# Kernel optimization log

Measured on AMD Instinct MI355X. Metric: run time of the kernel, lower is better.

The kernel has to match this reference:

```python
import jax, jax.numpy as jnp
import numpy as np

H = 8  # num_attention_heads
DH = 64  # attention_head_size
D = H * DH  # hidden_size = 512
LN_EPS = 1e-6


def setup_inputs() -> dict:
    key = jax.random.key(0)
    ks = jax.random.split(key, 12)
    B, L = 32, 196
    s = 1.0 / np.sqrt(D)
    return {
        "query_states": jax.random.normal(ks[0], (B, L, D), jnp.float32),
        "key_states": jax.random.normal(ks[1], (B, L, D), jnp.float32),
        "value_states": jax.random.normal(ks[2], (B, L, D), jnp.float32),
        "Wq": jax.random.normal(ks[3], (D, D), jnp.float32) * s,
        "bq": jnp.zeros((D,), jnp.float32),
        "Wk": jax.random.normal(ks[4], (D, D), jnp.float32) * s,
        "bk": jnp.zeros((D,), jnp.float32),
        "Wv": jax.random.normal(ks[5], (D, D), jnp.float32) * s,
        "bv": jnp.zeros((D,), jnp.float32),
        "ln_gamma": jnp.ones((D,), jnp.float32),
        "ln_beta": jnp.zeros((D,), jnp.float32),
        "logit_scale": jnp.ones((), jnp.float32),
    }


def _heads(x):
    # (B, L, D) -> (B, H, L, DH)
    B, L, _ = x.shape
    return x.reshape(B, L, H, DH).transpose(0, 2, 1, 3)


def reference(query_states, key_states, value_states, Wq, bq, Wk, bk, Wv, bv,
              ln_gamma, ln_beta, logit_scale):
    B, L, _ = query_states.shape
    q = _heads(query_states @ Wq.T + bq)  # (B,H,L,DH)
    k = _heads(key_states @ Wk.T + bk)
    v = _heads(value_states @ Wv.T + bv)

    # cross-batch retrieval: sum over heads and head_dim -> (a,b,l,m)
    retrieve = jnp.einsum('ahld,bhmd->ablm', q, k)
    mask_sum = jnp.float32(L)  # mask is all-ones (B, L)
    t2v = retrieve.max(axis=-1).sum(axis=2) / mask_sum  # (a,b)
    v2t = retrieve.max(axis=-2).sum(axis=2) / mask_sum  # (a,b)
    retrieve_logits = jnp.exp(logit_scale) * (t2v + v2t) / 2.0

    # self-attention (dropout is identity in eval)
    scores = jnp.einsum('bhld,bhmd->bhlm', q, k) / jnp.sqrt(jnp.float32(DH))
    probs = jax.nn.softmax(scores, axis=-1)  # (B,H,L,L)
    ctx = jnp.einsum('bhlm,bhmd->bhld', probs, v)
    ctx = ctx.transpose(0, 2, 1, 3).reshape(B, L, D)
    ctx = ctx + query_states

    mu = ctx.mean(axis=-1, keepdims=True)
    var = ((ctx - mu) ** 2).mean(axis=-1, keepdims=True)
    ctx = (ctx - mu) / jnp.sqrt(var + LN_EPS) * ln_gamma + ln_beta

    return ctx, retrieve_logits, probs.mean(axis=1)
```

## Files before the change

### kernel.cpp

```cpp
#include <hip/hip_runtime.h>
#include <hip/hip_bf16.h>

#define BB 32
#define LL 196
#define DD 512
#define HH 8
#define DHH 64
#define BL (BB*LL)
#define PVK 224
#define PSTR 236
#define ASTR 232

typedef __bf16 bf16x8 __attribute__((ext_vector_type(8)));
typedef float f32x4 __attribute__((ext_vector_type(4)));

#define MFMA16(a,b,c) __builtin_amdgcn_mfma_f32_16x16x32_bf16((a),(b),(c),0,0,0)

#define GLOAD_LDS16(g, l) __builtin_amdgcn_global_load_lds( \
    (const __attribute__((address_space(1))) void*)(g), \
    (__attribute__((address_space(3))) void*)(l), 16, 0, 0)

static __device__ __forceinline__ bf16x8 pack8(float4 v0, float4 v1) {
  bf16x8 o;
  o[0] = (__bf16)v0.x; o[1] = (__bf16)v0.y; o[2] = (__bf16)v0.z; o[3] = (__bf16)v0.w;
  o[4] = (__bf16)v1.x; o[5] = (__bf16)v1.y; o[6] = (__bf16)v1.z; o[7] = (__bf16)v1.w;
  return o;
}

static __device__ __forceinline__ unsigned fkey(float f) {
  unsigned u = __float_as_uint(f);
  return u ^ ((unsigned)((int)u >> 31) | 0x80000000u);
}
static __device__ __forceinline__ float unkey(unsigned k) {
  unsigned u = (k & 0x80000000u) ? (k ^ 0x80000000u) : ~k;
  return __uint_as_float(u);
}

#define STAGE_PAIR(SA, SB, abase, bbase) do { \
  const __bf16* aB_ = (abase); const __bf16* bB_ = (bbase); \
  _Pragma("unroll") \
  for (int c_ = 0; c_ < 4; ++c_) { \
    const int p_ = c_ * 256 + tid; \
    GLOAD_LDS16(aB_ + (size_t)(p_ >> 3) * DD + swoff, &SA[p_ * 8]); \
  } \
  _Pragma("unroll") \
  for (int c_ = 0; c_ < 4; ++c_) { \
    const int p_ = c_ * 256 + tid; \
    GLOAD_LDS16(bB_ + (size_t)(p_ >> 3) * DD + swoff, &SB[p_ * 8]); \
  } \
} while (0)

#define COMPUTE_TILE(SA, SB) do { \
  _Pragma("unroll") \
  for (int kc_ = 0; kc_ < 2; ++kc_) { \
    const int q_ = (((kc_ * 4 + (lane >> 4)) ^ (lane & 7)) << 3); \
    bf16x8 af_[4], bf_[4]; \
    _Pragma("unroll") \
    for (int mt_ = 0; mt_ < 4; ++mt_) \
      af_[mt_] = *(const bf16x8*)&SA[(wr + mt_ * 16 + (lane & 15)) * 64 + q_]; \
    _Pragma("unroll") \
    for (int nt_ = 0; nt_ < 4; ++nt_) \
      bf_[nt_] = *(const bf16x8*)&SB[(wc + nt_ * 16 + (lane & 15)) * 64 + q_]; \
    __builtin_amdgcn_s_setprio(1); \
    _Pragma("unroll") \
    for (int mt_ = 0; mt_ < 4; ++mt_) \
      _Pragma("unroll") \
      for (int nt_ = 0; nt_ < 4; ++nt_) \
        acc[mt_][nt_] = MFMA16(af_[mt_], bf_[nt_], acc[mt_][nt_]); \
    __builtin_amdgcn_s_setprio(0); \
  } \
} while (0)

__global__ __launch_bounds__(256) void cvt_kernel(
    const float* __restrict__ x0, const float* __restrict__ x1, const float* __restrict__ x2,
    const float* __restrict__ w0, const float* __restrict__ w1, const float* __restrict__ w2,
    __bf16* __restrict__ xb, __bf16* __restrict__ wb)
{
  const int z = blockIdx.y;
  const float* src; __bf16* dst; size_t i;
  if (blockIdx.x < 1568) {
    src = (z == 0) ? x0 : (z == 1) ? x1 : x2;
    dst = xb + (size_t)z * 3211264;
    i = (size_t)blockIdx.x * 256 + threadIdx.x;
  } else {
    src = (z == 0) ? w0 : (z == 1) ? w1 : w2;
    dst = wb + (size_t)z * 262144;
    i = (size_t)(blockIdx.x - 1568) * 256 + threadIdx.x;
  }
  const float4* s = (const float4*)(src + i * 8);
  float4 a = s[0], b = s[1];
  *(bf16x8*)(dst + i * 8) = pack8(a, b);
}

__global__ __launch_bounds__(256) void proj_gemm_kernel(
    const __bf16* __restrict__ xb, const __bf16* __restrict__ wb,
    const float* __restrict__ bq, const float* __restrict__ bk, const float* __restrict__ bv,
    __bf16* __restrict__ qp, __bf16* __restrict__ kp, __bf16* __restrict__ vp)
{
  __shared__ __bf16 sA0[128 * 64], sA1[128 * 64];
  __shared__ __bf16 sB0[128 * 64], sB1[128 * 64];

  const int z = blockIdx.z;
  const __bf16* A = xb + (size_t)z * 3211264;
  const __bf16* B = wb + (size_t)z * 262144;
  const float* bias = (z == 0) ? bq : (z == 1) ? bk : bv;
  __bf16* out = (z == 0) ? qp : (z == 1) ? kp : vp;

  const int tid = threadIdx.x;
  const int w = tid >> 6, lane = tid & 63;
  const int wr = (w >> 1) * 64, wc = (w & 1) * 64;
  const int bm = blockIdx.x * 128, bn = blockIdx.y * 128;
  const int swoff = ((tid & 7) ^ ((tid >> 3) & 7)) << 3;

  const __bf16* aP = A + (size_t)bm * DD;
  const __bf16* bP = B + (size_t)bn * DD;

  f32x4 acc[4][4] = {};

  STAGE_PAIR(sA0, sB0, aP, bP);
  __syncthreads();
  #pragma unroll
  for (int kt = 0; kt < 8; kt += 2) {
    if (kt + 1 < 8) STAGE_PAIR(sA1, sB1, aP + (kt + 1) * 64, bP + (kt + 1) * 64);
    COMPUTE_TILE(sA0, sB0);
    __syncthreads();
    if (kt + 2 < 8) STAGE_PAIR(sA0, sB0, aP + (kt + 2) * 64, bP + (kt + 2) * 64);
    COMPUTE_TILE(sA1, sB1);
    __syncthreads();
  }

  #pragma unroll
  for (int mt = 0; mt < 4; ++mt)
    #pragma unroll
    for (int nt = 0; nt < 4; ++nt)
      #pragma unroll
      for (int rr = 0; rr < 4; ++rr) {
        const int row = bm + wr + mt * 16 + (lane >> 4) * 4 + rr;
        const int col = bn + wc + nt * 16 + (lane & 15);
        out[(size_t)row * DD + col] = (__bf16)(acc[mt][nt][rr] + bias[col]);
      }
}

__global__ __launch_bounds__(256) void transpose_v_kernel(
    const __bf16* __restrict__ vp, __bf16* __restrict__ vpT)
{
  __shared__ __bf16 sT[64][72];
  const int bbh = blockIdx.x;
  const int mt = blockIdx.y;
  const int bb = bbh >> 3, h = bbh & 7;
  const int tid = threadIdx.x;
  {
    const int r = tid >> 2, c0 = (tid & 3) * 16;
    const int m = mt * 64 + r;
    bf16x8 z = {};
    bf16x8 v0 = z, v1 = z;
    if (m < LL) {
      const bf16x8* src = (const bf16x8*)&vp[(size_t)(bb * LL + m) * DD + h * DHH + c0];
      v0 = src[0]; v1 = src[1];
    }
    *(bf16x8*)&sT[r][c0]     = v0;
    *(bf16x8*)&sT[r][c0 + 8] = v1;
  }
  __syncthreads();
  {
    const int d = tid >> 2, mc0 = (tid & 3) * 16;
    if (mt * 64 + mc0 < PVK) {
      bf16x8 o0, o1;
      #pragma unroll
      for (int j = 0; j < 8; ++j) { o0[j] = sT[mc0 + j][d]; o1[j] = sT[mc0 + 8 + j][d]; }
      __bf16* dst = vpT + (size_t)(bbh * 64 + d) * PVK + mt * 64 + mc0;
      *(bf16x8*)dst = o0;
      *(bf16x8*)(dst + 8) = o1;
    }
  }
}

__global__ __launch_bounds__(256) void retrieve_kernel(
    const __bf16* __restrict__ qp, const __bf16* __restrict__ kp,
    unsigned* __restrict__ rmax, unsigned* __restrict__ cmax)
{
  __shared__ __bf16 sA0[128 * 64], sA1[128 * 64];
  __shared__ __bf16 sB0[128 * 64], sB1[128 * 64];

  const int orig = blockIdx.x;
  const int xcd = orig & 7, idx = orig >> 3;
  const int wg = (xcd == 0) ? idx : (301 + (xcd - 1) * 300 + idx);
  const int st = wg / 49, wi = wg % 49;
  const int brow = ((st / 7) * 7 + wi / 7) * 128;
  const int bcol = ((st % 7) * 7 + wi % 7) * 128;

  const int tid = threadIdx.x;
  const int w = tid >> 6, lane = tid & 63;
  const int wr = (w >> 1) * 64, wc = (w & 1) * 64;
  const int swoff = ((tid & 7) ^ ((tid >> 3) & 7)) << 3;

  const __bf16* aP = qp + (size_t)brow * DD;
  const __bf16* bP = kp + (size_t)bcol * DD;

  f32x4 acc[4][4] = {};

  STAGE_PAIR(sA0, sB0, aP, bP);
  __syncthreads();
  #pragma unroll
  for (int kt = 0; kt < 8; kt += 2) {
    if (kt + 1 < 8) STAGE_PAIR(sA1, sB1, aP + (kt + 1) * 64, bP + (kt + 1) * 64);
    COMPUTE_TILE(sA0, sB0);
    __syncthreads();
    if (kt + 2 < 8) STAGE_PAIR(sA0, sB0, aP + (kt + 2) * 64, bP + (kt + 2) * 64);
    COMPUTE_TILE(sA1, sB1);
    __syncthreads();
  }

  const int wcol0 = bcol + wc;
  const int wrow0 = brow + wr;
  {
    const int b0 = wcol0 / LL, b1 = (wcol0 + 63) / LL;
    for (int b = b0; b <= b1; ++b) {
      const int lo = b * LL, hi = lo + LL;
      #pragma unroll
      for (int mt = 0; mt < 4; ++mt)
        #pragma unroll
        for (int rr = 0; rr < 4; ++rr) {
          float m = -3e38f;
          #pragma unroll
          for (int nt = 0; nt < 4; ++nt) {
            const int col = wcol0 + nt * 16 + (lane & 15);
            if (col >= lo && col < hi) m = fmaxf(m, acc[mt][nt][rr]);
          }
          m = fmaxf(m, __shfl_xor(m, 1));
          m = fmaxf(m, __shfl_xor(m, 2));
          m = fmaxf(m, __shfl_xor(m, 4));
          m = fmaxf(m, __shfl_xor(m, 8));
          if ((lane & 15) == 0) {
            const int grow = wrow0 + mt * 16 + (lane >> 4) * 4 + rr;
            atomicMax(&rmax[(size_t)b * BL + grow], fkey(m));
          }
        }
    }
  }
  {
    const int a0 = wrow0 / LL, a1 = (wrow0 + 63) / LL;
    for (int a = a0; a <= a1; ++a) {
      const int lo = a * LL, hi = lo + LL;
      #pragma unroll
      for (int nt = 0; nt < 4; ++nt) {
        float cm = -3e38f;
        #pragma unroll
        for (int mt = 0; mt < 4; ++mt)
          #pragma unroll
          for (int rr = 0; rr < 4; ++rr) {
            const int grow = wrow0 + mt * 16 + (lane >> 4) * 4 + rr;
            if (grow >= lo && grow < hi) cm = fmaxf(cm, acc[mt][nt][rr]);
          }
        cm = fmaxf(cm, __shfl_xor(cm, 16));
        cm = fmaxf(cm, __shfl_xor(cm, 32));
        if (lane < 16) {
          const int col = wcol0 + nt * 16 + lane;
          atomicMax(&cmax[(size_t)a * BL + col], fkey(cm));
        }
      }
    }
  }
}

__global__ __launch_bounds__(256) void finish_kernel(
    const unsigned* __restrict__ rmax, const unsigned* __restrict__ cmax,
    const float* __restrict__ ls, float* __restrict__ out_logits)
{
  const int tid = threadIdx.x;
  const int w = tid >> 6, lane = tid & 63;
  const int pair = blockIdx.x * 4 + w;
  const int a = pair >> 5, b = pair & 31;
  float s = 0.f;
  #pragma unroll
  for (int k = 0; k < 4; ++k) {
    const int l = lane + k * 64;
    if (l < LL) {
      s += unkey(rmax[(size_t)b * BL + a * LL + l]);
      s += unkey(cmax[(size_t)a * BL + b * LL + l]);
    }
  }
  #pragma unroll
  for (int o = 1; o < 64; o <<= 1) s += __shfl_xor(s, o);
  if (lane == 0)
    out_logits[a * BB + b] = expf(ls[0]) * s * (0.5f / (float)LL);
}

__global__ __launch_bounds__(256) void attn_kernel(
    const __bf16* __restrict__ qp, const __bf16* __restrict__ kp,
    const __bf16* __restrict__ vpT, float* __restrict__ ctx,
    float* __restrict__ probs_out)
{
  __shared__ __bf16 pr[4][16][PSTR];
  __shared__ float pacc[16][ASTR];

  const int bb = blockIdx.x;
  const int strip = blockIdx.y;
  const int tid = threadIdx.x;
  const int w = tid >> 6, lane = tid & 63;
  const int row0 = strip * 16;

  for (int i = tid; i < 16 * ASTR; i += 256) ((float*)pacc)[i] = 0.f;
  for (int i = lane; i < 16 * 16; i += 64)
    pr[w][i >> 4][208 + (i & 15)] = (__bf16)0.f;
  __syncthreads();

  const int arow = row0 + (lane & 15);
  const bool aval = arow < LL;

  for (int rnd = 0; rnd < 2; ++rnd) {
    const int h = rnd * 4 + w;
    bf16x8 aq[2];
    #pragma unroll
    for (int kc = 0; kc < 2; ++kc) {
      bf16x8 z = {};
      aq[kc] = aval
        ? *(const bf16x8*)&qp[(size_t)(bb * LL + arow) * DD + h * DHH + kc * 32 + (lane >> 4) * 8]
        : z;
    }
    f32x4 s[13] = {};
    __builtin_amdgcn_s_setprio(1);
    #pragma unroll
    for (int nt = 0; nt < 13; ++nt) {
      const int brow = nt * 16 + (lane & 15);
      #pragma unroll
      for (int kc = 0; kc < 2; ++kc) {
        bf16x8 bk = {};
        if (brow < LL)
          bk = *(const bf16x8*)&kp[(size_t)(bb * LL + brow) * DD + h * DHH + kc * 32 + (lane >> 4) * 8];
        s[nt] = MFMA16(aq[kc], bk, s[nt]);
      }
    }
    __builtin_amdgcn_s_setprio(0);
    const int colbase = lane & 15;
    #pragma unroll
    for (int nt = 0; nt < 13; ++nt) {
      const bool cv = (nt * 16 + colbase) < LL;
      #pragma unroll
      for (int rr = 0; rr < 4; ++rr)
        s[nt][rr] = cv ? s[nt][rr] * 0.125f : -1e30f;
    }
    float mx[4], dn[4];
    #pragma unroll
    for (int rr = 0; rr < 4; ++rr) {
      float m = s[0][rr];
      #pragma unroll
      for (int nt = 1; nt < 13; ++nt) m = fmaxf(m, s[nt][rr]);
      m = fmaxf(m, __shfl_xor(m, 1));
      m = fmaxf(m, __shfl_xor(m, 2));
      m = fmaxf(m, __shfl_xor(m, 4));
      m = fmaxf(m, __shfl_xor(m, 8));
      mx[rr] = m;
    }
    #pragma unroll
    for (int nt = 0; nt < 13; ++nt)
      #pragma unroll
      for (int rr = 0; rr < 4; ++rr)
        s[nt][rr] = __expf(s[nt][rr] - mx[rr]);
    #pragma unroll
    for (int rr = 0; rr < 4; ++rr) {
      float d = 0.f;
      #pragma unroll
      for (int nt = 0; nt < 13; ++nt) d += s[nt][rr];
      d += __shfl_xor(d, 1);
      d += __shfl_xor(d, 2);
      d += __shfl_xor(d, 4);
      d += __shfl_xor(d, 8);
      dn[rr] = 1.f / d;
    }
    #pragma unroll
    for (int nt = 0; nt < 13; ++nt)
      #pragma unroll
      for (int rr = 0; rr < 4; ++rr)
        pr[w][(lane >> 4) * 4 + rr][nt * 16 + colbase] = (__bf16)(s[nt][rr] * dn[rr]);
    __syncthreads();

    f32x4 c4[4] = {};
    __builtin_amdgcn_s_setprio(1);
    #pragma unroll
    for (int kc = 0; kc < 7; ++kc) {
      bf16x8 ap = *(const bf16x8*)&pr[w][lane & 15][kc * 32 + (lane >> 4) * 8];
      #pragma unroll
      for (int dt = 0; dt < 4; ++dt) {
        bf16x8 bv = *(const bf16x8*)&vpT[(size_t)((bb * 8 + h) * 64 + dt * 16 + (lane & 15)) * PVK + kc * 32 + (lane >> 4) * 8];
        c4[dt] = MFMA16(ap, bv, c4[dt]);
      }
    }
    __builtin_amdgcn_s_setprio(0);
    #pragma unroll
    for (int dt = 0; dt < 4; ++dt)
      #pragma unroll
      for (int rr = 0; rr < 4; ++rr) {
        const int qrow = row0 + (lane >> 4) * 4 + rr;
        if (qrow < LL)
          ctx[(size_t)(bb * LL + qrow) * DD + h * DHH + dt * 16 + (lane & 15)] = c4[dt][rr];
      }
    {
      const int rr_ = tid >> 4;
      const int c0_ = (tid & 15) * 14;
      #pragma unroll
      for (int j = 0; j < 14; ++j) {
        const int c = c0_ + j;
        const float sum = (float)pr[0][rr_][c] + (float)pr[1][rr_][c]
                        + (float)pr[2][rr_][c] + (float)pr[3][rr_][c];
        pacc[rr_][c] += sum * 0.125f;
      }
    }
    __syncthreads();
  }

  const int rr_ = tid >> 4;
  const int qrow = row0 + rr_;
  if (qrow < LL) {
    #pragma unroll
    for (int j = 0; j < 13; ++j) {
      const int c = (tid & 15) + j * 16;
      if (c < LL)
        probs_out[((size_t)bb * LL + qrow) * LL + c] = pacc[rr_][c];
    }
  }
}

__global__ __launch_bounds__(256) void ln_kernel(
    float* __restrict__ ctx, const float* __restrict__ resid,
    const float* __restrict__ gamma, const float* __restrict__ beta)
{
  const int tid = threadIdx.x;
  const int w = tid >> 6, lane = tid & 63;
  const int row = blockIdx.x * 4 + w;
  float* crow = ctx + (size_t)row * DD;
  const float* rrow = resid + (size_t)row * DD;
  const int c = lane * 8;

  float4 a0 = *(const float4*)(crow + c);
  float4 a1 = *(const float4*)(crow + c + 4);
  float4 b0 = *(const float4*)(rrow + c);
  float4 b1 = *(const float4*)(rrow + c + 4);
  float v[8] = {a0.x + b0.x, a0.y + b0.y, a0.z + b0.z, a0.w + b0.w,
                a1.x + b1.x, a1.y + b1.y, a1.z + b1.z, a1.w + b1.w};

  float sum = 0.f;
  #pragma unroll
  for (int j = 0; j < 8; ++j) sum += v[j];
  #pragma unroll
  for (int o = 1; o < 64; o <<= 1) sum += __shfl_xor(sum, o);
  const float mu = sum * (1.f / (float)DD);

  float var = 0.f;
  #pragma unroll
  for (int j = 0; j < 8; ++j) { float d = v[j] - mu; var += d * d; }
  #pragma unroll
  for (int o = 1; o < 64; o <<= 1) var += __shfl_xor(var, o);
  const float rstd = rsqrtf(var * (1.f / (float)DD) + 1e-6f);

  float4 g0 = *(const float4*)(gamma + c);
  float4 g1 = *(const float4*)(gamma + c + 4);
  float4 e0 = *(const float4*)(beta + c);
  float4 e1 = *(const float4*)(beta + c + 4);
  float g[8] = {g0.x, g0.y, g0.z, g0.w, g1.x, g1.y, g1.z, g1.w};
  float e[8] = {e0.x, e0.y, e0.z, e0.w, e1.x, e1.y, e1.z, e1.w};

  float o_[8];
  #pragma unroll
  for (int j = 0; j < 8; ++j) o_[j] = (v[j] - mu) * rstd * g[j] + e[j];
  *(float4*)(crow + c)     = make_float4(o_[0], o_[1], o_[2], o_[3]);
  *(float4*)(crow + c + 4) = make_float4(o_[4], o_[5], o_[6], o_[7]);
}

extern "C" void kernel_launch(void* const* d_in, const int* in_sizes, int n_in,
                              void* d_out, int out_size, void* d_ws, size_t ws_size,
                              hipStream_t stream)
{
  const float* xq    = (const float*)d_in[0];
  const float* xk    = (const float*)d_in[1];
  const float* xv    = (const float*)d_in[2];
  const float* Wq    = (const float*)d_in[3];
  const float* bq    = (const float*)d_in[4];
  const float* Wk    = (const float*)d_in[5];
  const float* bk    = (const float*)d_in[6];
  const float* Wv    = (const float*)d_in[7];
  const float* bv    = (const float*)d_in[8];
  const float* gamma = (const float*)d_in[9];
  const float* beta  = (const float*)d_in[10];
  const float* ls    = (const float*)d_in[11];

  float* out_ctx    = (float*)d_out;
  float* out_logits = out_ctx + (size_t)BL * DD;
  float* out_probs  = out_logits + BB * BB;

  const size_t xsz = (size_t)BL * DD;
  const size_t wsz = (size_t)DD * DD;
  __bf16* xb = (__bf16*)d_ws;
  __bf16* wb = xb + 3 * xsz;
  __bf16* qp = wb + 3 * wsz;
  __bf16* kp = qp + xsz;
  __bf16* vp = kp + xsz;
  __bf16* vpT = xb;
  unsigned* rmax = (unsigned*)(xb + 3670016);
  unsigned* cmax = rmax + (size_t)BB * BL;

  cvt_kernel<<<dim3(1696, 3), 256, 0, stream>>>(xq, xk, xv, Wq, Wk, Wv, xb, wb);

  proj_gemm_kernel<<<dim3(49, 4, 3), 256, 0, stream>>>(xb, wb, bq, bk, bv, qp, kp, vp);

  transpose_v_kernel<<<dim3(BB * HH, 4), 256, 0, stream>>>(vp, vpT);

  hipMemsetAsync(rmax, 0, (size_t)2 * BB * BL * sizeof(unsigned), stream);

  retrieve_kernel<<<2401, 256, 0, stream>>>(qp, kp, rmax, cmax);
  finish_kernel<<<256, 256, 0, stream>>>(rmax, cmax, ls, out_logits);

  attn_kernel<<<dim3(BB, 13), 256, 0, stream>>>(qp, kp, vpT, out_ctx, out_probs);
  ln_kernel<<<BL / 4, 256, 0, stream>>>(out_ctx, xq, gamma, beta);
}
```

Measured before the change: 243.0 us.

## Single-buffer GEMM staging, drop setprio, widen attention to eight warps

The projection and retrieve GEMMs switch from double-buffered to single-buffered LDS staging, with a sync between load and compute, and the MFMA priority hints are removed. The attention kernel now uses 512 threads so each of the eight warps handles one head in a single pass. This replaces the two-round loop and removes the shared fp32 probability accumulator. The intent is lower LDS use and higher occupancy, but the GEMMs lose their load/compute overlap.

```diff
diff --git a/kernel.cpp b/kernel.cpp
--- a/kernel.cpp
+++ b/kernel.cpp
@@ -9,7 +9,6 @@
 #define BL (BB*LL)
 #define PVK 224
 #define PSTR 236
-#define ASTR 232
 
 typedef __bf16 bf16x8 __attribute__((ext_vector_type(8)));
 typedef float f32x4 __attribute__((ext_vector_type(4)));
@@ -61,13 +60,11 @@
     _Pragma("unroll") \
     for (int nt_ = 0; nt_ < 4; ++nt_) \
       bf_[nt_] = *(const bf16x8*)&SB[(wc + nt_ * 16 + (lane & 15)) * 64 + q_]; \
-    __builtin_amdgcn_s_setprio(1); \
     _Pragma("unroll") \
     for (int mt_ = 0; mt_ < 4; ++mt_) \
       _Pragma("unroll") \
       for (int nt_ = 0; nt_ < 4; ++nt_) \
         acc[mt_][nt_] = MFMA16(af_[mt_], bf_[nt_], acc[mt_][nt_]); \
-    __builtin_amdgcn_s_setprio(0); \
   } \
 } while (0)
 
@@ -97,8 +94,8 @@
     const float* __restrict__ bq, const float* __restrict__ bk, const float* __restrict__ bv,
     __bf16* __restrict__ qp, __bf16* __restrict__ kp, __bf16* __restrict__ vp)
 {
-  __shared__ __bf16 sA0[128 * 64], sA1[128 * 64];
-  __shared__ __bf16 sB0[128 * 64], sB1[128 * 64];
+  __shared__ __bf16 sA[128 * 64];
+  __shared__ __bf16 sB[128 * 64];
 
   const int z = blockIdx.z;
   const __bf16* A = xb + (size_t)z * 3211264;
@@ -117,15 +114,11 @@
 
   f32x4 acc[4][4] = {};
 
-  STAGE_PAIR(sA0, sB0, aP, bP);
-  __syncthreads();
-  #pragma unroll
-  for (int kt = 0; kt < 8; kt += 2) {
-    if (kt + 1 < 8) STAGE_PAIR(sA1, sB1, aP + (kt + 1) * 64, bP + (kt + 1) * 64);
-    COMPUTE_TILE(sA0, sB0);
+  #pragma unroll
+  for (int kt = 0; kt < 8; ++kt) {
+    STAGE_PAIR(sA, sB, aP + kt * 64, bP + kt * 64);
     __syncthreads();
-    if (kt + 2 < 8) STAGE_PAIR(sA0, sB0, aP + (kt + 2) * 64, bP + (kt + 2) * 64);
-    COMPUTE_TILE(sA1, sB1);
+    COMPUTE_TILE(sA, sB);
     __syncthreads();
   }
 
@@ -179,8 +172,8 @@
     const __bf16* __restrict__ qp, const __bf16* __restrict__ kp,
     unsigned* __restrict__ rmax, unsigned* __restrict__ cmax)
 {
-  __shared__ __bf16 sA0[128 * 64], sA1[128 * 64];
-  __shared__ __bf16 sB0[128 * 64], sB1[128 * 64];
+  __shared__ __bf16 sA[128 * 64];
+  __shared__ __bf16 sB[128 * 64];
 
   const int orig = blockIdx.x;
   const int xcd = orig & 7, idx = orig >> 3;
@@ -199,15 +192,11 @@
 
   f32x4 acc[4][4] = {};
 
-  STAGE_PAIR(sA0, sB0, aP, bP);
-  __syncthreads();
-  #pragma unroll
-  for (int kt = 0; kt < 8; kt += 2) {
-    if (kt + 1 < 8) STAGE_PAIR(sA1, sB1, aP + (kt + 1) * 64, bP + (kt + 1) * 64);
-    COMPUTE_TILE(sA0, sB0);
+  #pragma unroll
+  for (int kt = 0; kt < 8; ++kt) {
+    STAGE_PAIR(sA, sB, aP + kt * 64, bP + kt * 64);
     __syncthreads();
-    if (kt + 2 < 8) STAGE_PAIR(sA0, sB0, aP + (kt + 2) * 64, bP + (kt + 2) * 64);
-    COMPUTE_TILE(sA1, sB1);
+    COMPUTE_TILE(sA, sB);
     __syncthreads();
   }
 
@@ -286,137 +275,128 @@
     out_logits[a * BB + b] = expf(ls[0]) * s * (0.5f / (float)LL);
 }
 
-__global__ __launch_bounds__(256) void attn_kernel(
+__global__ __launch_bounds__(512) void attn_kernel(
     const __bf16* __restrict__ qp, const __bf16* __restrict__ kp,
     const __bf16* __restrict__ vpT, float* __restrict__ ctx,
     float* __restrict__ probs_out)
 {
-  __shared__ __bf16 pr[4][16][PSTR];
-  __shared__ float pacc[16][ASTR];
+  __shared__ __bf16 pr[8][16][PSTR];
 
   const int bb = blockIdx.x;
   const int strip = blockIdx.y;
   const int tid = threadIdx.x;
   const int w = tid >> 6, lane = tid & 63;
+  const int h = w;
   const int row0 = strip * 16;
 
-  for (int i = tid; i < 16 * ASTR; i += 256) ((float*)pacc)[i] = 0.f;
-  for (int i = lane; i < 16 * 16; i += 64)
+  for (int i = lane; i < 256; i += 64)
     pr[w][i >> 4][208 + (i & 15)] = (__bf16)0.f;
-  __syncthreads();
 
   const int arow = row0 + (lane & 15);
   const bool aval = arow < LL;
 
-  for (int rnd = 0; rnd < 2; ++rnd) {
-    const int h = rnd * 4 + w;
-    bf16x8 aq[2];
+  bf16x8 aq[2];
+  #pragma unroll
+  for (int kc = 0; kc < 2; ++kc) {
+    bf16x8 z = {};
+    aq[kc] = aval
+      ? *(const bf16x8*)&qp[(size_t)(bb * LL + arow) * DD + h * DHH + kc * 32 + (lane >> 4) * 8]
+      : z;
+  }
+  f32x4 s[13] = {};
+  __builtin_amdgcn_s_setprio(1);
+  #pragma unroll
+  for (int nt = 0; nt < 13; ++nt) {
+    const int brow = nt * 16 + (lane & 15);
     #pragma unroll
     for (int kc = 0; kc < 2; ++kc) {
-      bf16x8 z = {};
-      aq[kc] = aval
-        ? *(const bf16x8*)&qp[(size_t)(bb * LL + arow) * DD + h * DHH + kc * 32 + (lane >> 4) * 8]
-        : z;
-    }
-    f32x4 s[13] = {};
-    __builtin_amdgcn_s_setprio(1);
-    #pragma unroll
-    for (int nt = 0; nt < 13; ++nt) {
-      const int brow = nt * 16 + (lane & 15);
+      bf16x8 bk = {};
+      if (brow < LL)
+        bk = *(const bf16x8*)&kp[(size_t)(bb * LL + brow) * DD + h * DHH + kc * 32 + (lane >> 4) * 8];
+      s[nt] = MFMA16(aq[kc], bk, s[nt]);
+    }
+  }
+  __builtin_amdgcn_s_setprio(0);
+
+  const int colbase = lane & 15;
+  #pragma unroll
+  for (int nt = 0; nt < 13; ++nt) {
+    const bool cv = (nt * 16 + colbase) < LL;
+    #pragma unroll
+    for (int rr = 0; rr < 4; ++rr)
+      s[nt][rr] = cv ? s[nt][rr] * 0.125f : -1e30f;
+  }
+  float mx[4], dn[4];
+  #pragma unroll
+  for (int rr = 0; rr < 4; ++rr) {
+    float m = s[0][rr];
+    #pragma unroll
+    for (int nt = 1; nt < 13; ++nt) m = fmaxf(m, s[nt][rr]);
+    m = fmaxf(m, __shfl_xor(m, 1));
+    m = fmaxf(m, __shfl_xor(m, 2));
+    m = fmaxf(m, __shfl_xor(m, 4));
+    m = fmaxf(m, __shfl_xor(m, 8));
+    mx[rr] = m;
+  }
+  #pragma unroll
+  for (int nt = 0; nt < 13; ++nt)
+    #pragma unroll
+    for (int rr = 0; rr < 4; ++rr)
+      s[nt][rr] = __expf(s[nt][rr] - mx[rr]);
+  #pragma unroll
+  for (int rr = 0; rr < 4; ++rr) {
+    float d = 0.f;
+    #pragma unroll
+    for (int nt = 0; nt < 13; ++nt) d += s[nt][rr];
+    d += __shfl_xor(d, 1);
+    d += __shfl_xor(d, 2);
+    d += __shfl_xor(d, 4);
+    d += __shfl_xor(d, 8);
+    dn[rr] = 1.f / d;
+  }
+  #pragma unroll
+  for (int nt = 0; nt < 13; ++nt)
+    #pragma unroll
+    for (int rr = 0; rr < 4; ++rr)
+      pr[w][(lane >> 4) * 4 + rr][nt * 16 + colbase] = (__bf16)(s[nt][rr] * dn[rr]);
+  __syncthreads();
+
+  f32x4 c4[4] = {};
+  __builtin_amdgcn_s_setprio(1);
+  #pragma unroll
+  for (int kc = 0; kc < 7; ++kc) {
+    bf16x8 ap = *(const bf16x8*)&pr[w][lane & 15][kc * 32 + (lane >> 4) * 8];
+    #pragma unroll
+    for (int dt = 0; dt < 4; ++dt) {
+      bf16x8 bv = *(const bf16x8*)&vpT[(size_t)((bb * 8 + h) * 64 + dt * 16 + (lane & 15)) * PVK + kc * 32 + (lane >> 4) * 8];
+      c4[dt] = MFMA16(ap, bv, c4[dt]);
+    }
+  }
+  __builtin_amdgcn_s_setprio(0);
+  #pragma unroll
+  for (int dt = 0; dt < 4; ++dt)
+    #pragma unroll
+    for (int rr = 0; rr < 4; ++rr) {
+      const int qrow = row0 + (lane >> 4) * 4 + rr;
+      if (qrow < LL)
+        ctx[(size_t)(bb * LL + qrow) * DD + h * DHH + dt * 16 + (lane & 15)] = c4[dt][rr];
+    }
+
+  {
+    const int rr_ = tid >> 5;
+    const int c0_ = (tid & 31) * 7;
+    const int qrow = row0 + rr_;
+    if (qrow < LL) {
       #pragma unroll
-      for (int kc = 0; kc < 2; ++kc) {
-        bf16x8 bk = {};
-        if (brow < LL)
-          bk = *(const bf16x8*)&kp[(size_t)(bb * LL + brow) * DD + h * DHH + kc * 32 + (lane >> 4) * 8];
-        s[nt] = MFMA16(aq[kc], bk, s[nt]);
+      for (int j = 0; j < 7; ++j) {
+        const int c = c0_ + j;
+        if (c < LL) {
+          float sum = 0.f;
+          #pragma unroll
+          for (int ww = 0; ww < 8; ++ww) sum += (float)pr[ww][rr_][c];
+          probs_out[((size_t)bb * LL + qrow) * LL + c] = sum * 0.125f;
+        }
       }
-    }
-    __builtin_amdgcn_s_setprio(0);
-    const int colbase = lane & 15;
-    #pragma unroll
-    for (int nt = 0; nt < 13; ++nt) {
-      const bool cv = (nt * 16 + colbase) < LL;
-      #pragma unroll
-      for (int rr = 0; rr < 4; ++rr)
-        s[nt][rr] = cv ? s[nt][rr] * 0.125f : -1e30f;
-    }
-    float mx[4], dn[4];
-    #pragma unroll
-    for (int rr = 0; rr < 4; ++rr) {
-      float m = s[0][rr];
-      #pragma unroll
-      for (int nt = 1; nt < 13; ++nt) m = fmaxf(m, s[nt][rr]);
-      m = fmaxf(m, __shfl_xor(m, 1));
-      m = fmaxf(m, __shfl_xor(m, 2));
-      m = fmaxf(m, __shfl_xor(m, 4));
-      m = fmaxf(m, __shfl_xor(m, 8));
-      mx[rr] = m;
-    }
-    #pragma unroll
-    for (int nt = 0; nt < 13; ++nt)
-      #pragma unroll
-      for (int rr = 0; rr < 4; ++rr)
-        s[nt][rr] = __expf(s[nt][rr] - mx[rr]);
-    #pragma unroll
-    for (int rr = 0; rr < 4; ++rr) {
-      float d = 0.f;
-      #pragma unroll
-      for (int nt = 0; nt < 13; ++nt) d += s[nt][rr];
-      d += __shfl_xor(d, 1);
-      d += __shfl_xor(d, 2);
-      d += __shfl_xor(d, 4);
-      d += __shfl_xor(d, 8);
-      dn[rr] = 1.f / d;
-    }
-    #pragma unroll
-    for (int nt = 0; nt < 13; ++nt)
-      #pragma unroll
-      for (int rr = 0; rr < 4; ++rr)
-        pr[w][(lane >> 4) * 4 + rr][nt * 16 + colbase] = (__bf16)(s[nt][rr] * dn[rr]);
-    __syncthreads();
-
-    f32x4 c4[4] = {};
-    __builtin_amdgcn_s_setprio(1);
-    #pragma unroll
-    for (int kc = 0; kc < 7; ++kc) {
-      bf16x8 ap = *(const bf16x8*)&pr[w][lane & 15][kc * 32 + (lane >> 4) * 8];
-      #pragma unroll
-      for (int dt = 0; dt < 4; ++dt) {
-        bf16x8 bv = *(const bf16x8*)&vpT[(size_t)((bb * 8 + h) * 64 + dt * 16 + (lane & 15)) * PVK + kc * 32 + (lane >> 4) * 8];
-        c4[dt] = MFMA16(ap, bv, c4[dt]);
-      }
-    }
-    __builtin_amdgcn_s_setprio(0);
-    #pragma unroll
-    for (int dt = 0; dt < 4; ++dt)
-      #pragma unroll
-      for (int rr = 0; rr < 4; ++rr) {
-        const int qrow = row0 + (lane >> 4) * 4 + rr;
-        if (qrow < LL)
-          ctx[(size_t)(bb * LL + qrow) * DD + h * DHH + dt * 16 + (lane & 15)] = c4[dt][rr];
-      }
-    {
-      const int rr_ = tid >> 4;
-      const int c0_ = (tid & 15) * 14;
-      #pragma unroll
-      for (int j = 0; j < 14; ++j) {
-        const int c = c0_ + j;
-        const float sum = (float)pr[0][rr_][c] + (float)pr[1][rr_][c]
-                        + (float)pr[2][rr_][c] + (float)pr[3][rr_][c];
-        pacc[rr_][c] += sum * 0.125f;
-      }
-    }
-    __syncthreads();
-  }
-
-  const int rr_ = tid >> 4;
-  const int qrow = row0 + rr_;
-  if (qrow < LL) {
-    #pragma unroll
-    for (int j = 0; j < 13; ++j) {
-      const int c = (tid & 15) + j * 16;
-      if (c < LL)
-        probs_out[((size_t)bb * LL + qrow) * LL + c] = pacc[rr_][c];
     }
   }
 }
@@ -510,6 +490,6 @@
   retrieve_kernel<<<2401, 256, 0, stream>>>(qp, kp, rmax, cmax);
   finish_kernel<<<256, 256, 0, stream>>>(rmax, cmax, ls, out_logits);
 
-  attn_kernel<<<dim3(BB, 13), 256, 0, stream>>>(qp, kp, vpT, out_ctx, out_probs);
+  attn_kernel<<<dim3(BB, 13), 512, 0, stream>>>(qp, kp, vpT, out_ctx, out_probs);
   ln_kernel<<<BL / 4, 256, 0, stream>>>(out_ctx, xq, gamma, beta);
 }
```

Measured after the change: 237.7 us. -2.2%, faster.
